# Kernel tuning notes

Hardware: AMD Instinct MI355X
Metric: run time of the kernel (lower is better)

## Reference

```python
import jax, jax.numpy as jnp
import numpy as np

DIM = 2048
H = 256
N_HEADS = 4
HEAD_DIM = H // N_HEADS
N_SIG = 6
SW_HID = 2 * DIM  # SwiGLU(dim, dim*2)
B, S = 4, 2048
EPS = 1e-6


def _rmsnorm(v, w):
    return v * jax.lax.rsqrt(jnp.mean(v * v, axis=-1, keepdims=True) + EPS) * w


def setup_inputs() -> dict:
    key = jax.random.key(0)
    ks = jax.random.split(key, 32)
    sc = 0.02
    inp = {
        'x': jax.random.normal(ks[0], (B, S, DIM), jnp.float32),
        'epistemic': jax.random.uniform(ks[1], (B, 64), jnp.float32),
        'aleatoric': jax.random.uniform(ks[2], (B, 64), jnp.float32),
        'ood_score': jax.random.uniform(ks[3], (B,), jnp.float32),
        'conformal_unc': jax.random.uniform(ks[4], (B,), jnp.float32),
        'ece': jax.random.uniform(ks[5], (1,), jnp.float32),
        'moral_std': jax.random.uniform(ks[6], (B,), jnp.float32),
        # signal_proj: Linear(1, h)
        'sp_w': jax.random.normal(ks[7], (H, 1), jnp.float32) * sc,
        'sp_b': jnp.zeros((H,), jnp.float32),
        # MultiheadAttention packed qkv + out proj
        'in_proj_w': jax.random.normal(ks[8], (3 * H, H), jnp.float32) * sc,
        'in_proj_b': jnp.zeros((3 * H,), jnp.float32),
        'out_w': jax.random.normal(ks[9], (H, H), jnp.float32) * sc,
        'out_b': jnp.zeros((H,), jnp.float32),
        # confidence_head: Linear(6,h) -> GELU -> Linear(h,1) -> Sigmoid
        'ch_w1': jax.random.normal(ks[10], (H, N_SIG), jnp.float32) * sc,
        'ch_b1': jnp.zeros((H,), jnp.float32),
        'ch_w2': jax.random.normal(ks[11], (1, H), jnp.float32) * sc,
        'ch_b2': jnp.zeros((1,), jnp.float32),
        # summary_proj: Linear(h,dim) -> RMSNorm -> SwiGLU(dim, 2*dim) -> Linear(dim,dim) -> RMSNorm
        'sum_w1': jax.random.normal(ks[12], (DIM, H), jnp.float32) * sc,
        'sum_b1': jnp.zeros((DIM,), jnp.float32),
        'rms1_w': jnp.ones((DIM,), jnp.float32),
        'sw_w1': jax.random.normal(ks[13], (SW_HID, DIM), jnp.float32) * sc,
        'sw_w3': jax.random.normal(ks[14], (SW_HID, DIM), jnp.float32) * sc,
        'sw_w2': jax.random.normal(ks[15], (DIM, SW_HID), jnp.float32) * sc,
        'sum_w2': jax.random.normal(ks[16], (DIM, DIM), jnp.float32) * sc,
        'sum_b2': jnp.zeros((DIM,), jnp.float32),
        'rms2_w': jnp.ones((DIM,), jnp.float32),
        # final norm
        'norm_w': jnp.ones((DIM,), jnp.float32),
    }
    return inp


def reference(x, epistemic, aleatoric, ood_score, conformal_unc, ece, moral_std,
              sp_w, sp_b, in_proj_w, in_proj_b, out_w, out_b,
              ch_w1, ch_b1, ch_w2, ch_b2,
              sum_w1, sum_b1, rms1_w, sw_w1, sw_w3, sw_w2, sum_w2, sum_b2, rms2_w,
              norm_w):
    b, s, d = x.shape
    # [B, 6] stack of scalar uncertainty signals
    signals = jnp.stack([
        epistemic.mean(-1), aleatoric.mean(-1), ood_score, conformal_unc,
        jnp.broadcast_to(ece, (b,)), moral_std], axis=-1)
    # confidence head: Linear -> GELU(exact) -> Linear -> Sigmoid
    c = jax.nn.gelu(signals @ ch_w1.T + ch_b1, approximate=False)
    confidence = jax.nn.sigmoid(c @ ch_w2.T + ch_b2)[..., 0]
    # project each scalar signal to h dims: [B, 6, H]
    sp = signals[..., None] * sp_w[:, 0] + sp_b
    # self-attention over the 6 signal tokens
    qkv = sp @ in_proj_w.T + in_proj_b            # [B, 6, 3H]
    q, k, v = jnp.split(qkv, 3, axis=-1)
    q = q.reshape(b, N_SIG, N_HEADS, HEAD_DIM)
    k = k.reshape(b, N_SIG, N_HEADS, HEAD_DIM)
    v = v.reshape(b, N_SIG, N_HEADS, HEAD_DIM)
    scores = jnp.einsum('bqhd,bkhd->bhqk', q, k) / jnp.sqrt(jnp.float32(HEAD_DIM))
    attn = jax.nn.softmax(scores, axis=-1)
    o = jnp.einsum('bhqk,bkhd->bqhd', attn, v).reshape(b, N_SIG, H)
    o = o @ out_w.T + out_b
    unc_summary = o.mean(axis=1)                   # [B, H]
    # summary_proj applied (as in the original) to the [B*S, H] expanded rows
    u = jnp.broadcast_to(unc_summary[:, None, :], (b, s, H)).reshape(b * s, H)
    t = u @ sum_w1.T + sum_b1                      # [B*S, DIM]
    t = _rmsnorm(t, rms1_w)
    t = (jax.nn.silu(t @ sw_w1.T) * (t @ sw_w3.T)) @ sw_w2.T  # SwiGLU
    t = t @ sum_w2.T + sum_b2
    unc_embedding = _rmsnorm(t, rms2_w).reshape(b, s, d)
    x_aware = _rmsnorm(x + unc_embedding * 0.05, norm_w)
    return (x_aware, confidence, signals, unc_embedding)
```

## Files before the change

### kernel.cpp

```cpp
#include <hip/hip_runtime.h>
#include <math.h>

#define DIMN 2048
#define HDIM 256
#define NSIG 6
#define NHEADS 4
#define HEADDIM 64
#define SWHID 4096
#define BB 4
#define SSEQ 2048
#define EPSF 1e-6f

__device__ __forceinline__ float wsum(float v) {
    #pragma unroll
    for (int m = 1; m < 64; m <<= 1) v += __shfl_xor(v, m, 64);
    return v;
}

__device__ __forceinline__ float dot4(float4 a, float4 b) {
    return a.x*b.x + a.y*b.y + a.z*b.z + a.w*b.w;
}

__global__ __launch_bounds__(256) void k0_ac(
    const float* __restrict__ ipw, const float* __restrict__ ipb,
    const float* __restrict__ spw, const float* __restrict__ spb,
    float* __restrict__ A, float* __restrict__ C, float* __restrict__ accum)
{
    int t = threadIdx.x, wv = t >> 6, lane = t & 63;
    if (blockIdx.x == 0 && t < 8) accum[t] = 0.f;
    int r = blockIdx.x * 4 + wv;
    float4 w  = ((const float4*)(ipw + (size_t)r * HDIM))[lane];
    float4 a4 = ((const float4*)spw)[lane];
    float4 b4 = ((const float4*)spb)[lane];
    float aa = wsum(dot4(w, a4));
    float cc = wsum(dot4(w, b4));
    if (lane == 0) { A[r] = aa; C[r] = cc + ipb[r]; }
}

__global__ __launch_bounds__(256) void k1_attn(
    const float* __restrict__ epi, const float* __restrict__ ale,
    const float* __restrict__ ood, const float* __restrict__ cunc,
    const float* __restrict__ ece, const float* __restrict__ moral,
    const float* __restrict__ chw1, const float* __restrict__ chb1,
    const float* __restrict__ chw2, const float* __restrict__ chb2,
    const float* __restrict__ A, const float* __restrict__ C,
    float* __restrict__ obar, float* __restrict__ out_conf,
    float* __restrict__ out_sig)
{
    __shared__ float sSig[BB][NSIG];
    __shared__ float sA[768], sC[768];
    __shared__ float sQKV[NSIG][768];
    __shared__ float sAtt[NHEADS * NSIG][NSIG];
    __shared__ float sRed[256];
    int t = threadIdx.x;

    for (int r = t; r < 768; r += 256) { sA[r] = A[r]; sC[r] = C[r]; }
    if (t < BB * NSIG) {
        int b = t / NSIG, k = t - b * NSIG;
        float v;
        if (k == 0)      { float s = 0; for (int i = 0; i < 64; i++) s += epi[b*64+i]; v = s * (1.f/64.f); }
        else if (k == 1) { float s = 0; for (int i = 0; i < 64; i++) s += ale[b*64+i]; v = s * (1.f/64.f); }
        else if (k == 2) v = ood[b];
        else if (k == 3) v = cunc[b];
        else if (k == 4) v = ece[0];
        else             v = moral[b];
        sSig[b][k] = v;
        out_sig[t] = v;
    }
    __syncthreads();

    for (int b = 0; b < BB; b++) {
        float z = chb1[t];
        #pragma unroll
        for (int j = 0; j < NSIG; j++) z += sSig[b][j] * chw1[t * NSIG + j];
        float g = 0.5f * z * (1.f + erff(z * 0.70710678118654752f));
        sRed[t] = g * chw2[t];
        __syncthreads();
        for (int off = 128; off > 0; off >>= 1) {
            if (t < off) sRed[t] += sRed[t + off];
            __syncthreads();
        }
        if (t == 0) out_conf[b] = 1.f / (1.f + expf(-(sRed[0] + chb2[0])));
        __syncthreads();
    }

    for (int b = 0; b < BB; b++) {
        for (int idx = t; idx < NSIG * 768; idx += 256) {
            int j = idx / 768, r = idx - j * 768;
            sQKV[j][r] = sSig[b][j] * sA[r] + sC[r];
        }
        __syncthreads();
        if (t < NHEADS * NSIG) {
            int h = t / NSIG, qi = t - h * NSIG;
            float sc[NSIG]; float mx = -1e30f;
            for (int ki = 0; ki < NSIG; ki++) {
                float s = 0;
                for (int d = 0; d < HEADDIM; d++)
                    s += sQKV[qi][h*64 + d] * sQKV[ki][256 + h*64 + d];
                s *= 0.125f;
                sc[ki] = s; mx = fmaxf(mx, s);
            }
            float den = 0;
            for (int ki = 0; ki < NSIG; ki++) { sc[ki] = expf(sc[ki] - mx); den += sc[ki]; }
            float inv = 1.f / den;
            for (int ki = 0; ki < NSIG; ki++) sAtt[t][ki] = sc[ki] * inv;
        }
        __syncthreads();
        {
            int m = t, h = m >> 6;
            float ob = 0;
            for (int qi = 0; qi < NSIG; qi++) {
                float o = 0;
                #pragma unroll
                for (int ki = 0; ki < NSIG; ki++)
                    o += sAtt[h * NSIG + qi][ki] * sQKV[ki][512 + m];
                ob += o;
            }
            obar[b * HDIM + m] = ob * (1.f / 6.f);
        }
        __syncthreads();
    }
}

__global__ __launch_bounds__(256) void k1c_us(
    const float* __restrict__ obar, const float* __restrict__ outw,
    const float* __restrict__ outb, float* __restrict__ us)
{
    int t = threadIdx.x, wv = t >> 6, lane = t & 63;
    int m = blockIdx.x * 4 + wv;
    float4 w = ((const float4*)(outw + (size_t)m * HDIM))[lane];
    float acc[BB];
    #pragma unroll
    for (int b = 0; b < BB; b++) {
        float4 o = ((const float4*)(obar + b * HDIM))[lane];
        acc[b] = dot4(w, o);
    }
    #pragma unroll
    for (int b = 0; b < BB; b++) acc[b] = wsum(acc[b]);
    if (lane == 0) {
        float ob = outb[m];
        #pragma unroll
        for (int b = 0; b < BB; b++) us[b * HDIM + m] = acc[b] + ob;
    }
}

__global__ __launch_bounds__(256) void k2_sumproj(
    const float* __restrict__ us, const float* __restrict__ w1,
    const float* __restrict__ b1, const float* __restrict__ rw1,
    float* __restrict__ t1n, float* __restrict__ accum)
{
    __shared__ float bsq[BB];
    int t = threadIdx.x, wv = t >> 6, lane = t & 63;
    if (t < BB) bsq[t] = 0.f;
    __syncthreads();
    int d = blockIdx.x * 4 + wv;
    float4 w = ((const float4*)(w1 + (size_t)d * HDIM))[lane];
    float acc[BB];
    #pragma unroll
    for (int b = 0; b < BB; b++) {
        float4 u = ((const float4*)(us + b * HDIM))[lane];
        acc[b] = dot4(w, u);
    }
    #pragma unroll
    for (int b = 0; b < BB; b++) acc[b] = wsum(acc[b]);
    if (lane == 0) {
        #pragma unroll
        for (int b = 0; b < BB; b++) {
            float v = acc[b] + b1[d];
            atomicAdd(&bsq[b], v * v);
            t1n[b * DIMN + d] = v * rw1[d];
        }
    }
    __syncthreads();
    if (t < BB) atomicAdd(&accum[t], bsq[t]);
}

__global__ __launch_bounds__(256) void k3_swiglu(
    const float* __restrict__ t1n, const float* __restrict__ sw1,
    const float* __restrict__ sw3, const float* __restrict__ accum,
    float* __restrict__ h)
{
    __shared__ __align__(16) float sT[BB * DIMN];
    int t = threadIdx.x, wv = t >> 6, lane = t & 63;
    #pragma unroll
    for (int k = 0; k < 8; k++)
        ((float4*)sT)[k * 256 + t] = ((const float4*)t1n)[k * 256 + t];
    __syncthreads();
    int j = blockIdx.x * 4 + wv;
    const float4* r1 = (const float4*)(sw1 + (size_t)j * DIMN);
    const float4* r3 = (const float4*)(sw3 + (size_t)j * DIMN);
    float acc1[BB] = {0,0,0,0}, acc3[BB] = {0,0,0,0};
    #pragma unroll
    for (int it = 0; it < 8; it++) {
        float4 w1 = r1[it * 64 + lane];
        float4 w3 = r3[it * 64 + lane];
        #pragma unroll
        for (int b = 0; b < BB; b++) {
            float4 tv = ((const float4*)(sT + b * DIMN))[it * 64 + lane];
            acc1[b] += dot4(w1, tv);
            acc3[b] += dot4(w3, tv);
        }
    }
    #pragma unroll
    for (int b = 0; b < BB; b++) { acc1[b] = wsum(acc1[b]); acc3[b] = wsum(acc3[b]); }
    if (lane == 0) {
        #pragma unroll
        for (int b = 0; b < BB; b++) {
            float s = rsqrtf(accum[b] * (1.f / DIMN) + EPSF);
            float a = acc1[b] * s;
            float sil = a / (1.f + expf(-a));
            h[b * SWHID + j] = sil * (acc3[b] * s);
        }
    }
}

__global__ __launch_bounds__(256) void k4_down(
    const float* __restrict__ h, const float* __restrict__ sw2,
    float* __restrict__ t2)
{
    __shared__ __align__(16) float sH[BB * SWHID];
    int t = threadIdx.x, wv = t >> 6, lane = t & 63;
    #pragma unroll
    for (int k = 0; k < 16; k++)
        ((float4*)sH)[k * 256 + t] = ((const float4*)h)[k * 256 + t];
    __syncthreads();
    int d = blockIdx.x * 4 + wv;
    const float4* wr = (const float4*)(sw2 + (size_t)d * SWHID);
    float acc[BB] = {0,0,0,0};
    #pragma unroll
    for (int it = 0; it < 16; it++) {
        float4 w = wr[it * 64 + lane];
        #pragma unroll
        for (int b = 0; b < BB; b++) {
            float4 hv = ((const float4*)(sH + b * SWHID))[it * 64 + lane];
            acc[b] += dot4(w, hv);
        }
    }
    #pragma unroll
    for (int b = 0; b < BB; b++) acc[b] = wsum(acc[b]);
    if (lane == 0) {
        #pragma unroll
        for (int b = 0; b < BB; b++) t2[b * DIMN + d] = acc[b];
    }
}

__global__ __launch_bounds__(256) void k5_out(
    const float* __restrict__ t2, const float* __restrict__ w2,
    const float* __restrict__ b2, const float* __restrict__ rw2,
    float* __restrict__ t3n, float* __restrict__ accum)
{
    __shared__ __align__(16) float sT[BB * DIMN];
    __shared__ float bsq[BB];
    int t = threadIdx.x, wv = t >> 6, lane = t & 63;
    if (t < BB) bsq[t] = 0.f;
    #pragma unroll
    for (int k = 0; k < 8; k++)
        ((float4*)sT)[k * 256 + t] = ((const float4*)t2)[k * 256 + t];
    __syncthreads();
    int d = blockIdx.x * 4 + wv;
    const float4* wr = (const float4*)(w2 + (size_t)d * DIMN);
    float acc[BB] = {0,0,0,0};
    #pragma unroll
    for (int it = 0; it < 8; it++) {
        float4 w = wr[it * 64 + lane];
        #pragma unroll
        for (int b = 0; b < BB; b++) {
            float4 tv = ((const float4*)(sT + b * DIMN))[it * 64 + lane];
            acc[b] += dot4(w, tv);
        }
    }
    #pragma unroll
    for (int b = 0; b < BB; b++) acc[b] = wsum(acc[b]);
    if (lane == 0) {
        #pragma unroll
        for (int b = 0; b < BB; b++) {
            float v = acc[b] + b2[d];
            atomicAdd(&bsq[b], v * v);
            t3n[b * DIMN + d] = v * rw2[d];
        }
    }
    __syncthreads();
    if (t < BB) atomicAdd(&accum[4 + t], bsq[t]);
}

__global__ __launch_bounds__(256) void k7_final(
    const float* __restrict__ x, const float* __restrict__ t3n,
    const float* __restrict__ accum, const float* __restrict__ nw,
    float* __restrict__ xa, float* __restrict__ ue)
{
    __shared__ float sW[4];
    int t = threadIdx.x, wv = t >> 6, lane = t & 63;
    size_t row = blockIdx.x;
    int b = (int)(row >> 11);
    float scale2 = rsqrtf(accum[4 + b] * (1.f / DIMN) + EPSF);
    const float4* xr = (const float4*)(x + row * DIMN);
    const float4* tr = (const float4*)(t3n + (size_t)b * DIMN);
    float4 e[2], y[2];
    float ss = 0.f;
    #pragma unroll
    for (int k = 0; k < 2; k++) {
        int idx = k * 256 + t;
        float4 tv = tr[idx];
        float4 xv = xr[idx];
        e[k].x = tv.x * scale2; e[k].y = tv.y * scale2;
        e[k].z = tv.z * scale2; e[k].w = tv.w * scale2;
        y[k].x = xv.x + 0.05f * e[k].x; y[k].y = xv.y + 0.05f * e[k].y;
        y[k].z = xv.z + 0.05f * e[k].z; y[k].w = xv.w + 0.05f * e[k].w;
        ss += dot4(y[k], y[k]);
    }
    float wss = wsum(ss);
    if (lane == 0) sW[wv] = wss;
    __syncthreads();
    float rs = rsqrtf((sW[0] + sW[1] + sW[2] + sW[3]) * (1.f / DIMN) + EPSF);
    float4* xo = (float4*)(xa + row * DIMN);
    float4* uo = (float4*)(ue + row * DIMN);
    #pragma unroll
    for (int k = 0; k < 2; k++) {
        int idx = k * 256 + t;
        float4 nv = ((const float4*)nw)[idx];
        float4 o;
        o.x = y[k].x * rs * nv.x; o.y = y[k].y * rs * nv.y;
        o.z = y[k].z * rs * nv.z; o.w = y[k].w * rs * nv.w;
        xo[idx] = o;
        uo[idx] = e[k];
    }
}

extern "C" void kernel_launch(void* const* d_in, const int* in_sizes, int n_in,
                              void* d_out, int out_size, void* d_ws, size_t ws_size,
                              hipStream_t stream)
{
    (void)in_sizes; (void)n_in; (void)out_size; (void)ws_size;
    const float* x     = (const float*)d_in[0];
    const float* epi   = (const float*)d_in[1];
    const float* ale   = (const float*)d_in[2];
    const float* ood   = (const float*)d_in[3];
    const float* cunc  = (const float*)d_in[4];
    const float* ece   = (const float*)d_in[5];
    const float* moral = (const float*)d_in[6];
    const float* spw   = (const float*)d_in[7];
    const float* spb   = (const float*)d_in[8];
    const float* ipw   = (const float*)d_in[9];
    const float* ipb   = (const float*)d_in[10];
    const float* outw  = (const float*)d_in[11];
    const float* outb  = (const float*)d_in[12];
    const float* chw1  = (const float*)d_in[13];
    const float* chb1  = (const float*)d_in[14];
    const float* chw2  = (const float*)d_in[15];
    const float* chb2  = (const float*)d_in[16];
    const float* sumw1 = (const float*)d_in[17];
    const float* sumb1 = (const float*)d_in[18];
    const float* rms1  = (const float*)d_in[19];
    const float* sww1  = (const float*)d_in[20];
    const float* sww3  = (const float*)d_in[21];
    const float* sww2  = (const float*)d_in[22];
    const float* sumw2 = (const float*)d_in[23];
    const float* sumb2 = (const float*)d_in[24];
    const float* rms2  = (const float*)d_in[25];
    const float* normw = (const float*)d_in[26];

    float* out  = (float*)d_out;
    float* xa   = out;
    float* conf = out + (size_t)BB * SSEQ * DIMN;
    float* sig  = conf + BB;
    float* ue   = sig + BB * NSIG;

    float* ws    = (float*)d_ws;
    float* A     = ws;
    float* C     = ws + 768;
    float* obar  = ws + 1536;
    float* us    = ws + 2560;
    float* t1n   = ws + 3584;
    float* h     = ws + 11776;
    float* t2    = ws + 28160;
    float* t3n   = ws + 36352;
    float* accum = ws + 44544;

    k0_ac   <<<192, 256, 0, stream>>>(ipw, ipb, spw, spb, A, C, accum);
    k1_attn <<<1, 256, 0, stream>>>(epi, ale, ood, cunc, ece, moral,
                                    chw1, chb1, chw2, chb2, A, C, obar, conf, sig);
    k1c_us  <<<64, 256, 0, stream>>>(obar, outw, outb, us);
    k2_sumproj<<<512, 256, 0, stream>>>(us, sumw1, sumb1, rms1, t1n, accum);
    k3_swiglu <<<1024, 256, 0, stream>>>(t1n, sww1, sww3, accum, h);
    k4_down   <<<512, 256, 0, stream>>>(h, sww2, t2);
    k5_out    <<<512, 256, 0, stream>>>(t2, sumw2, sumb2, rms2, t3n, accum);
    k7_final  <<<8192, 256, 0, stream>>>(x, t3n, accum, normw, xa, ue);
}
```

Before: 366.5 us.

## Fuse front-end attention kernels into one and make final norm one-wave-per-row

Merges the A/C precompute, signal attention, confidence head and output projection into a single one-block kernel, which removes two launches and the global round trips for A, C and obar. The confidence head now reduces with wave shuffles instead of a shared-memory tree. The final RMSNorm kernel switches from one block per row to one wave per row, dropping the shared-memory reduction and the block barrier. The cost is that the fused front kernel runs the 768-row and 256-row GEMVs serially on one workgroup, which may lengthen that stage.

```diff
diff --git a/kernel.cpp b/kernel.cpp
--- a/kernel.cpp
+++ b/kernel.cpp
@@ -21,67 +21,73 @@
     return a.x*b.x + a.y*b.y + a.z*b.z + a.w*b.w;
 }
 
-__global__ __launch_bounds__(256) void k0_ac(
-    const float* __restrict__ ipw, const float* __restrict__ ipb,
-    const float* __restrict__ spw, const float* __restrict__ spb,
-    float* __restrict__ A, float* __restrict__ C, float* __restrict__ accum)
-{
-    int t = threadIdx.x, wv = t >> 6, lane = t & 63;
-    if (blockIdx.x == 0 && t < 8) accum[t] = 0.f;
-    int r = blockIdx.x * 4 + wv;
-    float4 w  = ((const float4*)(ipw + (size_t)r * HDIM))[lane];
-    float4 a4 = ((const float4*)spw)[lane];
-    float4 b4 = ((const float4*)spb)[lane];
-    float aa = wsum(dot4(w, a4));
-    float cc = wsum(dot4(w, b4));
-    if (lane == 0) { A[r] = aa; C[r] = cc + ipb[r]; }
-}
-
-__global__ __launch_bounds__(256) void k1_attn(
+__global__ __launch_bounds__(256) void kA_front(
     const float* __restrict__ epi, const float* __restrict__ ale,
     const float* __restrict__ ood, const float* __restrict__ cunc,
     const float* __restrict__ ece, const float* __restrict__ moral,
+    const float* __restrict__ ipw, const float* __restrict__ ipb,
+    const float* __restrict__ spw, const float* __restrict__ spb,
     const float* __restrict__ chw1, const float* __restrict__ chb1,
     const float* __restrict__ chw2, const float* __restrict__ chb2,
-    const float* __restrict__ A, const float* __restrict__ C,
-    float* __restrict__ obar, float* __restrict__ out_conf,
-    float* __restrict__ out_sig)
+    const float* __restrict__ outw, const float* __restrict__ outb,
+    float* __restrict__ us, float* __restrict__ out_conf,
+    float* __restrict__ out_sig, float* __restrict__ accum)
 {
     __shared__ float sSig[BB][NSIG];
     __shared__ float sA[768], sC[768];
     __shared__ float sQKV[NSIG][768];
     __shared__ float sAtt[NHEADS * NSIG][NSIG];
-    __shared__ float sRed[256];
-    int t = threadIdx.x;
-
-    for (int r = t; r < 768; r += 256) { sA[r] = A[r]; sC[r] = C[r]; }
-    if (t < BB * NSIG) {
-        int b = t / NSIG, k = t - b * NSIG;
-        float v;
-        if (k == 0)      { float s = 0; for (int i = 0; i < 64; i++) s += epi[b*64+i]; v = s * (1.f/64.f); }
-        else if (k == 1) { float s = 0; for (int i = 0; i < 64; i++) s += ale[b*64+i]; v = s * (1.f/64.f); }
-        else if (k == 2) v = ood[b];
-        else if (k == 3) v = cunc[b];
-        else if (k == 4) v = ece[0];
-        else             v = moral[b];
-        sSig[b][k] = v;
-        out_sig[t] = v;
-    }
-    __syncthreads();
-
-    for (int b = 0; b < BB; b++) {
-        float z = chb1[t];
-        #pragma unroll
-        for (int j = 0; j < NSIG; j++) z += sSig[b][j] * chw1[t * NSIG + j];
-        float g = 0.5f * z * (1.f + erff(z * 0.70710678118654752f));
-        sRed[t] = g * chw2[t];
-        __syncthreads();
-        for (int off = 128; off > 0; off >>= 1) {
-            if (t < off) sRed[t] += sRed[t + off];
-            __syncthreads();
-        }
-        if (t == 0) out_conf[b] = 1.f / (1.f + expf(-(sRed[0] + chb2[0])));
-        __syncthreads();
+    __shared__ float sObar[BB][HDIM];
+    __shared__ float sRedW[BB][4];
+    int t = threadIdx.x, wv = t >> 6, lane = t & 63;
+
+    if (t < 8) accum[t] = 0.f;
+
+    {
+        int b = wv;
+        float e = epi[b * 64 + lane];
+        float a = ale[b * 64 + lane];
+        float se = wsum(e) * (1.f / 64.f);
+        float sa = wsum(a) * (1.f / 64.f);
+        if (lane == 0) {
+            sSig[b][0] = se; sSig[b][1] = sa;
+            sSig[b][2] = ood[b]; sSig[b][3] = cunc[b];
+            sSig[b][4] = ece[0]; sSig[b][5] = moral[b];
+            for (int k = 0; k < NSIG; k++) out_sig[b * NSIG + k] = sSig[b][k];
+        }
+    }
+
+    {
+        float4 spw4 = ((const float4*)spw)[lane];
+        float4 spb4 = ((const float4*)spb)[lane];
+        for (int r = wv; r < 768; r += 4) {
+            float4 w = ((const float4*)(ipw + (size_t)r * HDIM))[lane];
+            float aa = wsum(dot4(w, spw4));
+            float cc = wsum(dot4(w, spb4));
+            if (lane == 0) { sA[r] = aa; sC[r] = cc + ipb[r]; }
+        }
+    }
+    __syncthreads();
+
+    {
+        float c1[NSIG];
+        #pragma unroll
+        for (int j = 0; j < NSIG; j++) c1[j] = chw1[t * NSIG + j];
+        float cb = chb1[t], cw2 = chw2[t];
+        #pragma unroll
+        for (int b = 0; b < BB; b++) {
+            float z = cb;
+            #pragma unroll
+            for (int j = 0; j < NSIG; j++) z += sSig[b][j] * c1[j];
+            float g = 0.5f * z * (1.f + erff(z * 0.70710678118654752f));
+            float v = wsum(g * cw2);
+            if (lane == 0) sRedW[b][wv] = v;
+        }
+    }
+    __syncthreads();
+    if (t < BB) {
+        float s = sRedW[t][0] + sRedW[t][1] + sRedW[t][2] + sRedW[t][3] + chb2[0];
+        out_conf[t] = 1.f / (1.f + expf(-s));
     }
 
     for (int b = 0; b < BB; b++) {
@@ -116,31 +122,26 @@
                     o += sAtt[h * NSIG + qi][ki] * sQKV[ki][512 + m];
                 ob += o;
             }
-            obar[b * HDIM + m] = ob * (1.f / 6.f);
+            sObar[b][m] = ob * (1.f / 6.f);
         }
         __syncthreads();
     }
-}
-
-__global__ __launch_bounds__(256) void k1c_us(
-    const float* __restrict__ obar, const float* __restrict__ outw,
-    const float* __restrict__ outb, float* __restrict__ us)
-{
-    int t = threadIdx.x, wv = t >> 6, lane = t & 63;
-    int m = blockIdx.x * 4 + wv;
-    float4 w = ((const float4*)(outw + (size_t)m * HDIM))[lane];
-    float acc[BB];
-    #pragma unroll
-    for (int b = 0; b < BB; b++) {
-        float4 o = ((const float4*)(obar + b * HDIM))[lane];
-        acc[b] = dot4(w, o);
-    }
-    #pragma unroll
-    for (int b = 0; b < BB; b++) acc[b] = wsum(acc[b]);
-    if (lane == 0) {
-        float ob = outb[m];
-        #pragma unroll
-        for (int b = 0; b < BB; b++) us[b * HDIM + m] = acc[b] + ob;
+
+    {
+        float4 ob4[BB];
+        #pragma unroll
+        for (int b = 0; b < BB; b++) ob4[b] = ((const float4*)sObar[b])[lane];
+        for (int m = wv; m < HDIM; m += 4) {
+            float4 w = ((const float4*)(outw + (size_t)m * HDIM))[lane];
+            float acc[BB];
+            #pragma unroll
+            for (int b = 0; b < BB; b++) acc[b] = wsum(dot4(w, ob4[b]));
+            if (lane == 0) {
+                float o = outb[m];
+                #pragma unroll
+                for (int b = 0; b < BB; b++) us[b * HDIM + m] = acc[b] + o;
+            }
+        }
     }
 }
 
@@ -288,18 +289,17 @@
     const float* __restrict__ accum, const float* __restrict__ nw,
     float* __restrict__ xa, float* __restrict__ ue)
 {
-    __shared__ float sW[4];
-    int t = threadIdx.x, wv = t >> 6, lane = t & 63;
-    size_t row = blockIdx.x;
+    int t = threadIdx.x, wv = t >> 6, lane = t & 63;
+    size_t row = (size_t)blockIdx.x * 4 + wv;
     int b = (int)(row >> 11);
     float scale2 = rsqrtf(accum[4 + b] * (1.f / DIMN) + EPSF);
     const float4* xr = (const float4*)(x + row * DIMN);
     const float4* tr = (const float4*)(t3n + (size_t)b * DIMN);
-    float4 e[2], y[2];
+    float4 e[8], y[8];
     float ss = 0.f;
     #pragma unroll
-    for (int k = 0; k < 2; k++) {
-        int idx = k * 256 + t;
+    for (int k = 0; k < 8; k++) {
+        int idx = k * 64 + lane;
         float4 tv = tr[idx];
         float4 xv = xr[idx];
         e[k].x = tv.x * scale2; e[k].y = tv.y * scale2;
@@ -308,15 +308,12 @@
         y[k].z = xv.z + 0.05f * e[k].z; y[k].w = xv.w + 0.05f * e[k].w;
         ss += dot4(y[k], y[k]);
     }
-    float wss = wsum(ss);
-    if (lane == 0) sW[wv] = wss;
-    __syncthreads();
-    float rs = rsqrtf((sW[0] + sW[1] + sW[2] + sW[3]) * (1.f / DIMN) + EPSF);
+    float rs = rsqrtf(wsum(ss) * (1.f / DIMN) + EPSF);
     float4* xo = (float4*)(xa + row * DIMN);
     float4* uo = (float4*)(ue + row * DIMN);
     #pragma unroll
-    for (int k = 0; k < 2; k++) {
-        int idx = k * 256 + t;
+    for (int k = 0; k < 8; k++) {
+        int idx = k * 64 + lane;
         float4 nv = ((const float4*)nw)[idx];
         float4 o;
         o.x = y[k].x * rs * nv.x; o.y = y[k].y * rs * nv.y;
@@ -366,23 +363,19 @@
     float* ue   = sig + BB * NSIG;
 
     float* ws    = (float*)d_ws;
-    float* A     = ws;
-    float* C     = ws + 768;
-    float* obar  = ws + 1536;
-    float* us    = ws + 2560;
-    float* t1n   = ws + 3584;
-    float* h     = ws + 11776;
-    float* t2    = ws + 28160;
-    float* t3n   = ws + 36352;
-    float* accum = ws + 44544;
-
-    k0_ac   <<<192, 256, 0, stream>>>(ipw, ipb, spw, spb, A, C, accum);
-    k1_attn <<<1, 256, 0, stream>>>(epi, ale, ood, cunc, ece, moral,
-                                    chw1, chb1, chw2, chb2, A, C, obar, conf, sig);
-    k1c_us  <<<64, 256, 0, stream>>>(obar, outw, outb, us);
+    float* us    = ws;
+    float* t1n   = ws + 1024;
+    float* h     = ws + 9216;
+    float* t2    = ws + 25600;
+    float* t3n   = ws + 33792;
+    float* accum = ws + 41984;
+
+    kA_front  <<<1, 256, 0, stream>>>(epi, ale, ood, cunc, ece, moral,
+                                      ipw, ipb, spw, spb, chw1, chb1, chw2, chb2,
+                                      outw, outb, us, conf, sig, accum);
     k2_sumproj<<<512, 256, 0, stream>>>(us, sumw1, sumb1, rms1, t1n, accum);
     k3_swiglu <<<1024, 256, 0, stream>>>(t1n, sww1, sww3, accum, h);
     k4_down   <<<512, 256, 0, stream>>>(h, sww2, t2);
     k5_out    <<<512, 256, 0, stream>>>(t2, sumw2, sumb2, rms2, t3n, accum);
-    k7_final  <<<8192, 256, 0, stream>>>(x, t3n, accum, normw, xa, ue);
-}
+    k7_final  <<<2048, 256, 0, stream>>>(x, t3n, accum, normw, xa, ue);
+}
```

Result: slower. 609.4 us (+66.3%).
